# Kernel tuning notes

Hardware: AMD Instinct MI355X
Metric: run time of the kernel (lower is better)

## Reference

```python
import jax, jax.numpy as jnp
import numpy as np

B, L, D, H, FF, NS = 4, 1024, 1024, 16, 4096, 64
HD = D // H
EPS = 1e-5


def layer_norm(x, g, b):
    mu = jnp.mean(x, axis=-1, keepdims=True)
    var = jnp.mean(jnp.square(x - mu), axis=-1, keepdims=True)
    return (x - mu) * jax.lax.rsqrt(var + EPS) * g + b


def mha(xq, xkv, wqkv, bqkv, wo, bo, bias=None):
    # torch nn.MultiheadAttention with packed in_proj: rows [0:D]=Q, [D:2D]=K, [2D:3D]=V
    Bq, Lq, Dm = xq.shape
    q = (xq @ wqkv[:Dm].T + bqkv[:Dm]).reshape(Bq, Lq, H, HD).transpose(0, 2, 1, 3)
    k = (xkv @ wqkv[Dm:2 * Dm].T + bqkv[Dm:2 * Dm]).reshape(Bq, -1, H, HD).transpose(0, 2, 1, 3)
    v = (xkv @ wqkv[2 * Dm:].T + bqkv[2 * Dm:]).reshape(Bq, -1, H, HD).transpose(0, 2, 1, 3)
    scores = jnp.einsum('bhqd,bhkd->bhqk', q, k) / np.sqrt(HD).astype(np.float32)
    if bias is not None:
        scores = scores + bias.reshape(Bq, H, Lq, -1)
    attn = jax.nn.softmax(scores, axis=-1)
    out = jnp.einsum('bhqk,bhkd->bhqd', attn, v).transpose(0, 2, 1, 3).reshape(Bq, Lq, Dm)
    return out @ wo.T + bo


def setup_inputs() -> dict:
    key = jax.random.key(0)
    ks = jax.random.split(key, 16)
    w = lambda k, shape: jax.random.normal(k, shape, jnp.float32) * 0.02
    return {
        'x': jax.random.normal(ks[0], (B, L, D), jnp.float32),
        'alibi_bias': jax.random.normal(ks[1], (B * H, L, L), jnp.float32) * 0.1,
        'species_emb': jax.random.normal(ks[2], (B, NS, D), jnp.float32),
        'norm1_g': jnp.ones(D), 'norm1_b': jnp.zeros(D),
        'sa_wqkv': w(ks[3], (3 * D, D)), 'sa_bqkv': jnp.zeros(3 * D),
        'sa_wo': w(ks[4], (D, D)), 'sa_bo': jnp.zeros(D),
        'ca_nq_g': jnp.ones(D), 'ca_nq_b': jnp.zeros(D),
        'ca_nkv_g': jnp.ones(D), 'ca_nkv_b': jnp.zeros(D),
        'ca_wqkv': w(ks[5], (3 * D, D)), 'ca_bqkv': jnp.zeros(3 * D),
        'ca_wo': w(ks[6], (D, D)), 'ca_bo': jnp.zeros(D),
        'gate_param': jnp.float32(0.1),
        'ffn_g': jnp.ones(D), 'ffn_b': jnp.zeros(D),
        'ffn_w1': w(ks[7], (2 * FF, D)), 'ffn_b1': jnp.zeros(2 * FF),
        'ffn_w2': w(ks[8], (D, FF)), 'ffn_b2': jnp.zeros(D),
    }


def reference(x, alibi_bias, species_emb,
              norm1_g, norm1_b, sa_wqkv, sa_bqkv, sa_wo, sa_bo,
              ca_nq_g, ca_nq_b, ca_nkv_g, ca_nkv_b, ca_wqkv, ca_bqkv, ca_wo, ca_bo,
              gate_param, ffn_g, ffn_b, ffn_w1, ffn_b1, ffn_w2, ffn_b2):
    # 1) pre-norm self-attention with ALiBi additive bias
    h = layer_norm(x, norm1_g, norm1_b)
    h = mha(h, h, sa_wqkv, sa_bqkv, sa_wo, sa_bo, bias=alibi_bias)
    x = x + h  # dropout is identity in eval mode
    # 2) gated cross-attention with species embeddings
    q = layer_norm(x, ca_nq_g, ca_nq_b)
    kv = layer_norm(species_emb, ca_nkv_g, ca_nkv_b)
    cross = mha(q, kv, ca_wqkv, ca_bqkv, ca_wo, ca_bo)
    x = x + jax.nn.sigmoid(gate_param) * cross
    # 3) GEGLU feed-forward
    f = layer_norm(x, ffn_g, ffn_b) @ ffn_w1.T + ffn_b1
    val, gate = f[..., :FF], f[..., FF:]
    f = (val * jax.nn.gelu(gate, approximate=False)) @ ffn_w2.T + ffn_b2
    return x + f
```

## Files before the change

kernel.cpp:

```cpp
#include <hip/hip_runtime.h>
#include <hip/hip_bf16.h>
#include <cstdint>

#define DEVI __device__ __forceinline__

typedef __attribute__((ext_vector_type(8))) short  short8;
typedef __attribute__((ext_vector_type(8))) __bf16 bf16x8;
typedef __attribute__((ext_vector_type(4))) float  f32x4;

DEVI float bf2f(short s) {
    unsigned u = ((unsigned)(unsigned short)s) << 16;
    return __builtin_bit_cast(float, u);
}
DEVI short f2bf(float f) {
    unsigned u = __builtin_bit_cast(unsigned, f);
    u = u + 0x7FFF + ((u >> 16) & 1);
    return (short)(u >> 16);
}

__global__ __launch_bounds__(256) void cvt_bf16(const float* src, short* dst, long n) {
    const long i = ((long)blockIdx.x * 256 + threadIdx.x) * 8;
    const float4 a = *(const float4*)&src[i];
    const float4 b = *(const float4*)&src[i + 4];
    short8 o;
    o[0] = f2bf(a.x); o[1] = f2bf(a.y); o[2] = f2bf(a.z); o[3] = f2bf(a.w);
    o[4] = f2bf(b.x); o[5] = f2bf(b.y); o[6] = f2bf(b.z); o[7] = f2bf(b.w);
    *(short8*)&dst[i] = o;
}

struct GArgs {
    const short* A; long lda, sAb, sAh;
    const short* B; long ldb, sBb, sBh;
    short* C;       long ldc, sCb, sCh;
    const float* bias;
    const float* addm; long ldad, sDb, sDh;
    float* resid;
    float* outf;
    const float* gate;
    const float* addf;
    float scale;
    int K, nh;
};

template<int BM, int BN, int EPI>
__global__ __launch_bounds__(256) void gemm_bt(GArgs a) {
    constexpr int WM = BM / 2, WN = BN / 2, MI = WM / 16, NI = WN / 16;
    __shared__ __align__(16) short As[BM * 32];
    __shared__ __align__(16) short Bs[BN * 32];
    const int tid = threadIdx.x;
    const int wave = tid >> 6, lane = tid & 63;
    const int wm = (wave >> 1) * WM, wn = (wave & 1) * WN;
    const int q = lane >> 4, r = lane & 15;
    const long bb = blockIdx.z / a.nh, hh = blockIdx.z % a.nh;
    const short* Ab = a.A + bb * a.sAb + hh * a.sAh + (long)blockIdx.y * BM * a.lda;
    const short* Bb = a.B + bb * a.sBb + hh * a.sBh + (long)blockIdx.x * BN * a.ldb;
    const int trow = tid >> 2;
    const int tcol = (tid & 3) * 8;
    f32x4 acc[MI][NI] = {};

    for (int k0 = 0; k0 < a.K; k0 += 32) {
        __syncthreads();
#pragma unroll
        for (int i = 0; i < BM / 64; i++) {
            const short* g = Ab + (long)(i * 64 + trow) * a.lda + k0 + tcol;
            __builtin_amdgcn_global_load_lds(
                (const __attribute__((address_space(1))) void*)g,
                (__attribute__((address_space(3))) void*)&As[(i * 64 + trow) * 32 + tcol],
                16, 0, 0);
        }
#pragma unroll
        for (int i = 0; i < BN / 64; i++) {
            const short* g = Bb + (long)(i * 64 + trow) * a.ldb + k0 + tcol;
            __builtin_amdgcn_global_load_lds(
                (const __attribute__((address_space(1))) void*)g,
                (__attribute__((address_space(3))) void*)&Bs[(i * 64 + trow) * 32 + tcol],
                16, 0, 0);
        }
        asm volatile("s_waitcnt vmcnt(0)" ::: "memory");
        __syncthreads();
        bf16x8 av[MI], bv[NI];
#pragma unroll
        for (int mi = 0; mi < MI; mi++)
            av[mi] = __builtin_bit_cast(bf16x8, *(const short8*)&As[(wm + mi * 16 + r) * 32 + q * 8]);
#pragma unroll
        for (int ni = 0; ni < NI; ni++)
            bv[ni] = __builtin_bit_cast(bf16x8, *(const short8*)&Bs[(wn + ni * 16 + r) * 32 + q * 8]);
#pragma unroll
        for (int mi = 0; mi < MI; mi++)
#pragma unroll
            for (int ni = 0; ni < NI; ni++)
                acc[mi][ni] = __builtin_amdgcn_mfma_f32_16x16x32_bf16(av[mi], bv[ni], acc[mi][ni], 0, 0, 0);
    }

    const long m0 = (long)blockIdx.y * BM + wm;
    const long n0 = (long)blockIdx.x * BN + wn;
    float gs = a.scale;
    if (EPI == 2 && a.gate) gs *= 1.f / (1.f + __expf(-(*a.gate)));
#pragma unroll
    for (int mi = 0; mi < MI; mi++)
#pragma unroll
        for (int ni = 0; ni < NI; ni++)
#pragma unroll
            for (int j = 0; j < 4; j++) {
                const long m = m0 + mi * 16 + q * 4 + j;
                const long n = n0 + ni * 16 + r;
                float v = acc[mi][ni][j];
                if constexpr (EPI == 0) {
                    if (a.bias) v += a.bias[n];
                    a.C[bb * a.sCb + hh * a.sCh + m * a.ldc + n] = f2bf(v);
                } else if constexpr (EPI == 1) {
                    v *= a.scale;
                    if (a.addm) v += a.addm[bb * a.sDb + hh * a.sDh + m * a.ldad + n];
                    a.C[bb * a.sCb + hh * a.sCh + m * a.ldc + n] = f2bf(v);
                } else if constexpr (EPI == 2) {
                    if (a.bias) v += a.bias[n];
                    const long idx = m * a.ldc + n;
                    const float base = a.addf ? a.addf[idx] : a.resid[idx];
                    a.resid[idx] = base + gs * v;
                } else {
                    if (a.bias) v += a.bias[n];
                    a.outf[m * a.ldc + n] = a.resid[m * a.ldc + n] + v;
                }
            }
}

__global__ __launch_bounds__(256) void flash_sa(const short* qkv, const short* vt,
                                                const float* alibi, short* Obuf) {
    __shared__ __align__(16) short Qs[64 * 64], Ks[64 * 64], Vs[64 * 64], Ps[64 * 64];
    const int tid = threadIdx.x;
    const int wave = tid >> 6, lane = tid & 63, q = lane >> 4, r = lane & 15;
    const int qt = blockIdx.x, bh = blockIdx.y, b = bh >> 4, h = bh & 15;
    const long qrow0 = (long)b * 1024 + qt * 64;
    const int rw = tid >> 3, sp = tid & 7;

#pragma unroll
    for (int i = 0; i < 2; i++) {
        const int row = i * 32 + rw;
        const int c8 = (sp ^ (row & 7)) * 8;
        const short* g = qkv + (qrow0 + row) * 3072 + h * 64 + c8;
        __builtin_amdgcn_global_load_lds(
            (const __attribute__((address_space(1))) void*)g,
            (__attribute__((address_space(3))) void*)&Qs[row * 64 + sp * 8], 16, 0, 0);
    }

    f32x4 o[4] = {};
    float m_run[4], l_run[4];
#pragma unroll
    for (int j = 0; j < 4; j++) { m_run[j] = -1e30f; l_run[j] = 0.f; }

    for (int kt = 0; kt < 16; kt++) {
        __syncthreads();
#pragma unroll
        for (int i = 0; i < 2; i++) {
            const int row = i * 32 + rw;
            const int c8 = (sp ^ (row & 7)) * 8;
            const short* gk = qkv + ((long)b * 1024 + kt * 64 + row) * 3072 + 1024 + h * 64 + c8;
            __builtin_amdgcn_global_load_lds(
                (const __attribute__((address_space(1))) void*)gk,
                (__attribute__((address_space(3))) void*)&Ks[row * 64 + sp * 8], 16, 0, 0);
            const short* gv = vt + ((long)bh * 64 + row) * 1024 + kt * 64 + c8;
            __builtin_amdgcn_global_load_lds(
                (const __attribute__((address_space(1))) void*)gv,
                (__attribute__((address_space(3))) void*)&Vs[row * 64 + sp * 8], 16, 0, 0);
        }
        float al[4][4];
        const float* ab = alibi + (long)bh * 1048576 + (long)(qt * 64 + wave * 16) * 1024 + kt * 64;
#pragma unroll
        for (int ni = 0; ni < 4; ni++)
#pragma unroll
            for (int j = 0; j < 4; j++)
                al[ni][j] = ab[(q * 4 + j) * 1024 + ni * 16 + r];
        asm volatile("s_waitcnt vmcnt(0)" ::: "memory");
        __syncthreads();

        f32x4 sacc[4] = {};
        const int arow = wave * 16 + r;
#pragma unroll
        for (int kk = 0; kk < 2; kk++) {
            const bf16x8 av = __builtin_bit_cast(bf16x8,
                *(const short8*)&Qs[arow * 64 + (((kk * 4 + q) ^ (arow & 7)) * 8)]);
#pragma unroll
            for (int ni = 0; ni < 4; ni++) {
                const int brow = ni * 16 + r;
                const bf16x8 bv = __builtin_bit_cast(bf16x8,
                    *(const short8*)&Ks[brow * 64 + (((kk * 4 + q) ^ (brow & 7)) * 8)]);
                sacc[ni] = __builtin_amdgcn_mfma_f32_16x16x32_bf16(av, bv, sacc[ni], 0, 0, 0);
            }
        }
        float s[4][4];
#pragma unroll
        for (int ni = 0; ni < 4; ni++)
#pragma unroll
            for (int j = 0; j < 4; j++)
                s[ni][j] = sacc[ni][j] * 0.125f + al[ni][j];

        float p[4][4];
#pragma unroll
        for (int j = 0; j < 4; j++) {
            float mx = fmaxf(fmaxf(s[0][j], s[1][j]), fmaxf(s[2][j], s[3][j]));
#pragma unroll
            for (int off = 8; off; off >>= 1) mx = fmaxf(mx, __shfl_xor(mx, off));
            const float newm = fmaxf(m_run[j], mx);
            const float sc = __expf(m_run[j] - newm);
            m_run[j] = newm;
            float rs = 0.f;
#pragma unroll
            for (int ni = 0; ni < 4; ni++) { p[ni][j] = __expf(s[ni][j] - newm); rs += p[ni][j]; }
#pragma unroll
            for (int off = 8; off; off >>= 1) rs += __shfl_xor(rs, off);
            l_run[j] = l_run[j] * sc + rs;
#pragma unroll
            for (int nd = 0; nd < 4; nd++) o[nd][j] *= sc;
        }

#pragma unroll
        for (int ni = 0; ni < 4; ni++)
#pragma unroll
            for (int j = 0; j < 4; j++) {
                const int row = wave * 16 + q * 4 + j;
                const int col = ni * 16 + r;
                const int scol = (((col >> 3) ^ (row & 7)) << 3) | (col & 7);
                Ps[row * 64 + scol] = f2bf(p[ni][j]);
            }
        asm volatile("s_waitcnt lgkmcnt(0)" ::: "memory");

        const int prow = wave * 16 + r;
#pragma unroll
        for (int kk = 0; kk < 2; kk++) {
            const bf16x8 pa = __builtin_bit_cast(bf16x8,
                *(const short8*)&Ps[prow * 64 + (((kk * 4 + q) ^ (prow & 7)) * 8)]);
#pragma unroll
            for (int nd = 0; nd < 4; nd++) {
                const int vrow = nd * 16 + r;
                const bf16x8 vv = __builtin_bit_cast(bf16x8,
                    *(const short8*)&Vs[vrow * 64 + (((kk * 4 + q) ^ (vrow & 7)) * 8)]);
                o[nd] = __builtin_amdgcn_mfma_f32_16x16x32_bf16(pa, vv, o[nd], 0, 0, 0);
            }
        }
    }

#pragma unroll
    for (int nd = 0; nd < 4; nd++)
#pragma unroll
        for (int j = 0; j < 4; j++) {
            const long m = qrow0 + wave * 16 + q * 4 + j;
            Obuf[m * 1024 + h * 64 + nd * 16 + r] = f2bf(o[nd][j] / l_run[j]);
        }
}

__global__ __launch_bounds__(256) void ln_rows(const float* X, const float* gw,
                                               const float* bw, short* Y) {
    const long row = blockIdx.x;
    const float* x = X + row * 1024;
    const int t = threadIdx.x;
    float v[4], s1 = 0.f, s2 = 0.f;
#pragma unroll
    for (int i = 0; i < 4; i++) {
        v[i] = x[t + i * 256];
        s1 += v[i]; s2 += v[i] * v[i];
    }
#pragma unroll
    for (int o = 32; o; o >>= 1) { s1 += __shfl_xor(s1, o); s2 += __shfl_xor(s2, o); }
    __shared__ float sm[8];
    if ((t & 63) == 0) { sm[t >> 6] = s1; sm[4 + (t >> 6)] = s2; }
    __syncthreads();
    s1 = sm[0] + sm[1] + sm[2] + sm[3];
    s2 = sm[4] + sm[5] + sm[6] + sm[7];
    const float mu = s1 * (1.f / 1024.f);
    const float var = s2 * (1.f / 1024.f) - mu * mu;
    const float rr = rsqrtf(var + 1e-5f);
#pragma unroll
    for (int i = 0; i < 4; i++) {
        const int c = t + i * 256;
        Y[row * 1024 + c] = f2bf((v[i] - mu) * rr * gw[c] + bw[c]);
    }
}

__global__ __launch_bounds__(256) void softmax1024(short* S) {
    const long row = blockIdx.x;
    short* p = S + row * 1024;
    const int t = threadIdx.x;
    float v[4];
#pragma unroll
    for (int i = 0; i < 4; i++) v[i] = bf2f(p[t + i * 256]);
    float m = fmaxf(fmaxf(v[0], v[1]), fmaxf(v[2], v[3]));
#pragma unroll
    for (int o = 32; o; o >>= 1) m = fmaxf(m, __shfl_xor(m, o));
    __shared__ float sm[4];
    if ((t & 63) == 0) sm[t >> 6] = m;
    __syncthreads();
    m = fmaxf(fmaxf(sm[0], sm[1]), fmaxf(sm[2], sm[3]));
    float e[4], s = 0.f;
#pragma unroll
    for (int i = 0; i < 4; i++) { e[i] = __expf(v[i] - m); s += e[i]; }
#pragma unroll
    for (int o = 32; o; o >>= 1) s += __shfl_xor(s, o);
    __syncthreads();
    if ((t & 63) == 0) sm[t >> 6] = s;
    __syncthreads();
    s = sm[0] + sm[1] + sm[2] + sm[3];
    const float inv = 1.f / s;
#pragma unroll
    for (int i = 0; i < 4; i++) p[t + i * 256] = f2bf(e[i] * inv);
}

__global__ __launch_bounds__(256) void softmax64(short* S) {
    const long row = (long)blockIdx.x * 4 + (threadIdx.x >> 6);
    const int lane = threadIdx.x & 63;
    short* p = S + row * 64;
    float v = bf2f(p[lane]);
    float m = v;
#pragma unroll
    for (int o = 32; o; o >>= 1) m = fmaxf(m, __shfl_xor(m, o));
    float e = __expf(v - m), s = e;
#pragma unroll
    for (int o = 32; o; o >>= 1) s += __shfl_xor(s, o);
    p[lane] = f2bf(e / s);
}

__global__ __launch_bounds__(256) void transpose_v_sa(const short* qkv, short* vt) {
    __shared__ short tbuf[64][68];
    const int j0 = blockIdx.x * 64, h = blockIdx.y, b = blockIdx.z;
    const int tid = threadIdx.x;
#pragma unroll
    for (int i = 0; i < 16; i++) {
        const int idx = i * 256 + tid, jj = idx >> 6, hd = idx & 63;
        tbuf[jj][hd] = qkv[(long)(b * 1024 + j0 + jj) * 3072 + 2048 + h * 64 + hd];
    }
    __syncthreads();
    const long bh = b * 16 + h;
#pragma unroll
    for (int i = 0; i < 16; i++) {
        const int idx = i * 256 + tid, hd = idx >> 6, jj = idx & 63;
        vt[(bh * 64 + hd) * 1024 + j0 + jj] = tbuf[jj][hd];
    }
}

__global__ __launch_bounds__(256) void transpose_v_ca(const short* kv2, short* vt2) {
    __shared__ short tbuf[64][68];
    const int bh = blockIdx.x, b = bh >> 4, h = bh & 15;
    const int tid = threadIdx.x;
#pragma unroll
    for (int i = 0; i < 16; i++) {
        const int idx = i * 256 + tid, jj = idx >> 6, hd = idx & 63;
        tbuf[jj][hd] = kv2[(long)(b * 64 + jj) * 2048 + 1024 + h * 64 + hd];
    }
    __syncthreads();
#pragma unroll
    for (int i = 0; i < 16; i++) {
        const int idx = i * 256 + tid, hd = idx >> 6, jj = idx & 63;
        vt2[((long)bh * 64 + hd) * 64 + jj] = tbuf[jj][hd];
    }
}

__global__ __launch_bounds__(256) void geglu_inplace(short* f1) {
    const long i = (long)blockIdx.x * 256 + threadIdx.x;
    const long m = i >> 9, j8 = (i & 511) * 8;
    const short8 av = *(const short8*)&f1[m * 8192 + j8];
    const short8 gv = *(const short8*)&f1[m * 8192 + 4096 + j8];
    short8 o;
#pragma unroll
    for (int jj = 0; jj < 8; jj++) {
        const float xv = bf2f(av[jj]), gg = bf2f(gv[jj]);
        const float ge = 0.5f * gg * (1.f + erff(gg * 0.7071067811865476f));
        o[jj] = f2bf(xv * ge);
    }
    *(short8*)&f1[m * 8192 + j8] = o;
}

extern "C" void kernel_launch(void* const* d_in, const int* in_sizes, int n_in,
                              void* d_out, int out_size, void* d_ws, size_t ws_size,
                              hipStream_t stream) {
    const float* x        = (const float*)d_in[0];
    const float* alibi    = (const float*)d_in[1];
    const float* species  = (const float*)d_in[2];
    const float* n1g      = (const float*)d_in[3];
    const float* n1b      = (const float*)d_in[4];
    const float* sa_wqkv  = (const float*)d_in[5];
    const float* sa_bqkv  = (const float*)d_in[6];
    const float* sa_wo    = (const float*)d_in[7];
    const float* sa_bo    = (const float*)d_in[8];
    const float* ca_nq_g  = (const float*)d_in[9];
    const float* ca_nq_b  = (const float*)d_in[10];
    const float* ca_nkv_g = (const float*)d_in[11];
    const float* ca_nkv_b = (const float*)d_in[12];
    const float* ca_wqkv  = (const float*)d_in[13];
    const float* ca_bqkv  = (const float*)d_in[14];
    const float* ca_wo    = (const float*)d_in[15];
    const float* ca_bo    = (const float*)d_in[16];
    const float* gate     = (const float*)d_in[17];
    const float* ffn_g    = (const float*)d_in[18];
    const float* ffn_b    = (const float*)d_in[19];
    const float* ffn_w1   = (const float*)d_in[20];
    const float* ffn_b1   = (const float*)d_in[21];
    const float* ffn_w2   = (const float*)d_in[22];
    const float* ffn_b2   = (const float*)d_in[23];
    float* out = (float*)d_out;

    const dim3 blk(256);
    char* ws = (char*)d_ws;

    if (ws_size >= (304ull << 20)) {
        float* resid  = (float*)(ws);
        short* lnbuf  = (short*)(ws + (16l << 20));
        short* Obuf   = (short*)(ws + (24l << 20));
        short* vt     = (short*)(ws + (32l << 20));
        short* qkv    = (short*)(ws + (40l << 20));
        short* w_saq  = (short*)(ws + (64l << 20));
        short* w_sawo = (short*)(ws + (70l << 20));
        short* w_caq  = (short*)(ws + (72l << 20));
        short* w_cawo = (short*)(ws + (78l << 20));
        short* w_f1   = (short*)(ws + (80l << 20));
        short* w_f2   = (short*)(ws + (96l << 20));
        short* kv2    = (short*)(ws + (104l << 20));
        short* Sbuf   = (short*)(ws + (112l << 20));
        short* f1     = (short*)(ws + (240l << 20));

        cvt_bf16<<<1536, blk, 0, stream>>>(sa_wqkv, w_saq, 3145728);
        cvt_bf16<<<512,  blk, 0, stream>>>(sa_wo,   w_sawo, 1048576);
        cvt_bf16<<<1536, blk, 0, stream>>>(ca_wqkv, w_caq, 3145728);
        cvt_bf16<<<512,  blk, 0, stream>>>(ca_wo,   w_cawo, 1048576);
        cvt_bf16<<<4096, blk, 0, stream>>>(ffn_w1,  w_f1, 8388608);
        cvt_bf16<<<2048, blk, 0, stream>>>(ffn_w2,  w_f2, 4194304);

        ln_rows<<<4096, blk, 0, stream>>>(x, n1g, n1b, lnbuf);

        {
            GArgs a{}; a.A = lnbuf; a.lda = 1024; a.B = w_saq; a.ldb = 1024;
            a.C = qkv; a.ldc = 3072; a.bias = sa_bqkv; a.K = 1024; a.nh = 1; a.scale = 1.f;
            gemm_bt<128, 128, 0><<<dim3(24, 32, 1), blk, 0, stream>>>(a);
        }
        transpose_v_sa<<<dim3(16, 16, 4), blk, 0, stream>>>(qkv, vt);

        flash_sa<<<dim3(16, 64), blk, 0, stream>>>(qkv, vt, alibi, Obuf);

        {
            GArgs a{}; a.A = Obuf; a.lda = 1024; a.B = w_sawo; a.ldb = 1024;
            a.ldc = 1024; a.bias = sa_bo; a.resid = resid; a.addf = x;
            a.scale = 1.f; a.K = 1024; a.nh = 1;
            gemm_bt<128, 64, 2><<<dim3(16, 32, 1), blk, 0, stream>>>(a);
        }

        ln_rows<<<4096, blk, 0, stream>>>(resid, ca_nq_g, ca_nq_b, lnbuf);
        {
            GArgs a{}; a.A = lnbuf; a.lda = 1024; a.B = w_caq; a.ldb = 1024;
            a.C = qkv; a.ldc = 1024; a.bias = ca_bqkv; a.K = 1024; a.nh = 1; a.scale = 1.f;
            gemm_bt<128, 64, 0><<<dim3(16, 32, 1), blk, 0, stream>>>(a);
        }
        ln_rows<<<256, blk, 0, stream>>>(species, ca_nkv_g, ca_nkv_b, lnbuf);
        {
            GArgs a{}; a.A = lnbuf; a.lda = 1024; a.B = w_caq + 1024 * 1024; a.ldb = 1024;
            a.C = kv2; a.ldc = 2048; a.bias = ca_bqkv + 1024; a.K = 1024; a.nh = 1; a.scale = 1.f;
            gemm_bt<128, 128, 0><<<dim3(16, 2, 1), blk, 0, stream>>>(a);
        }
        transpose_v_ca<<<64, blk, 0, stream>>>(kv2, vt);
        {
            GArgs a{}; a.A = qkv; a.lda = 1024; a.sAb = 1048576; a.sAh = 64;
            a.B = kv2; a.ldb = 2048; a.sBb = 131072; a.sBh = 64;
            a.C = Sbuf; a.ldc = 64; a.sCb = 1048576; a.sCh = 65536;
            a.scale = 0.125f; a.K = 64; a.nh = 16;
            gemm_bt<64, 64, 1><<<dim3(1, 16, 64), blk, 0, stream>>>(a);
        }
        softmax64<<<16384, blk, 0, stream>>>(Sbuf);
        {
            GArgs a{}; a.A = Sbuf; a.lda = 64; a.sAb = 1048576; a.sAh = 65536;
            a.B = vt; a.ldb = 64; a.sBb = 65536; a.sBh = 4096;
            a.C = Obuf; a.ldc = 1024; a.sCb = 1048576; a.sCh = 64;
            a.K = 64; a.nh = 16; a.scale = 1.f;
            gemm_bt<64, 64, 0><<<dim3(1, 16, 64), blk, 0, stream>>>(a);
        }
        {
            GArgs a{}; a.A = Obuf; a.lda = 1024; a.B = w_cawo; a.ldb = 1024;
            a.ldc = 1024; a.bias = ca_bo; a.resid = resid; a.gate = gate;
            a.scale = 1.f; a.K = 1024; a.nh = 1;
            gemm_bt<128, 64, 2><<<dim3(16, 32, 1), blk, 0, stream>>>(a);
        }

        ln_rows<<<4096, blk, 0, stream>>>(resid, ffn_g, ffn_b, lnbuf);
        {
            GArgs a{}; a.A = lnbuf; a.lda = 1024; a.B = w_f1; a.ldb = 1024;
            a.C = f1; a.ldc = 8192; a.bias = ffn_b1; a.K = 1024; a.nh = 1; a.scale = 1.f;
            gemm_bt<128, 128, 0><<<dim3(64, 32, 1), blk, 0, stream>>>(a);
        }
        geglu_inplace<<<8192, blk, 0, stream>>>(f1);
        {
            GArgs a{}; a.A = f1; a.lda = 8192; a.B = w_f2; a.ldb = 4096;
            a.ldc = 1024; a.bias = ffn_b2; a.resid = resid; a.outf = out;
            a.scale = 1.f; a.K = 4096; a.nh = 1;
            gemm_bt<128, 64, 3><<<dim3(16, 32, 1), blk, 0, stream>>>(a);
        }
        return;
    }

    float* resid  = (float*)(ws);
    short* lnbuf  = (short*)(ws + (16l << 20));
    short* Obuf   = (short*)(ws + (24l << 20));
    short* vt     = (short*)(ws + (32l << 20));
    short* qkv    = (short*)(ws + (40l << 20));
    short* Sbuf   = (short*)(ws + (64l << 20));
    short* f1     = Sbuf;
    short* kv2    = qkv + 4194304;
    short* w_sawo = (short*)(ws + (80l << 20));
    short* w_caq  = (short*)(ws + (82l << 20));
    short* w_cawo = (short*)(ws + (88l << 20));
    short* w_saq  = (short*)(ws + (90l << 20));
    short* w_f1   = qkv;
    short* w_f2   = (short*)(ws + (56l << 20));

    cvt_bf16<<<1536, blk, 0, stream>>>(sa_wqkv, w_saq, 3145728);
    cvt_bf16<<<512,  blk, 0, stream>>>(sa_wo,   w_sawo, 1048576);
    cvt_bf16<<<1536, blk, 0, stream>>>(ca_wqkv, w_caq, 3145728);
    cvt_bf16<<<512,  blk, 0, stream>>>(ca_wo,   w_cawo, 1048576);

    hipMemcpyAsync(resid, x, (size_t)4194304 * 4, hipMemcpyDeviceToDevice, stream);
    ln_rows<<<4096, blk, 0, stream>>>(x, n1g, n1b, lnbuf);

    {
        GArgs a{}; a.A = lnbuf; a.lda = 1024; a.B = w_saq; a.ldb = 1024;
        a.C = qkv; a.ldc = 3072; a.bias = sa_bqkv; a.K = 1024; a.nh = 1; a.scale = 1.f;
        gemm_bt<128, 128, 0><<<dim3(24, 32, 1), blk, 0, stream>>>(a);
    }
    transpose_v_sa<<<dim3(16, 16, 4), blk, 0, stream>>>(qkv, vt);

    for (int c = 0; c < 8; c++) {
        const int b = c >> 1, hc = c & 1;
        const long boff = (long)b * 1024 * 3072;
        {
            GArgs a{}; a.A = qkv + boff + hc * 512; a.lda = 3072; a.sAh = 64;
            a.B = qkv + boff + 1024 + hc * 512; a.ldb = 3072; a.sBh = 64;
            a.C = Sbuf; a.ldc = 1024; a.sCh = 1048576;
            a.addm = alibi + ((long)(b * 16 + hc * 8)) * 1048576; a.ldad = 1024; a.sDh = 1048576;
            a.scale = 0.125f; a.K = 64; a.nh = 8;
            gemm_bt<128, 128, 1><<<dim3(8, 8, 8), blk, 0, stream>>>(a);
        }
        softmax1024<<<8192, blk, 0, stream>>>(Sbuf);
        {
            GArgs a{}; a.A = Sbuf; a.lda = 1024; a.sAh = 1048576;
            a.B = vt + (long)b * 1048576 + (long)hc * 8 * 65536; a.ldb = 1024; a.sBh = 65536;
            a.C = Obuf + (long)b * 1048576 + hc * 512; a.ldc = 1024; a.sCh = 64;
            a.K = 1024; a.nh = 8; a.scale = 1.f;
            gemm_bt<64, 64, 0><<<dim3(1, 16, 8), blk, 0, stream>>>(a);
        }
    }
    {
        GArgs a{}; a.A = Obuf; a.lda = 1024; a.B = w_sawo; a.ldb = 1024;
        a.ldc = 1024; a.bias = sa_bo; a.resid = resid; a.scale = 1.f; a.K = 1024; a.nh = 1;
        gemm_bt<128, 128, 2><<<dim3(8, 32, 1), blk, 0, stream>>>(a);
    }

    ln_rows<<<4096, blk, 0, stream>>>(resid, ca_nq_g, ca_nq_b, lnbuf);
    {
        GArgs a{}; a.A = lnbuf; a.lda = 1024; a.B = w_caq; a.ldb = 1024;
        a.C = qkv; a.ldc = 1024; a.bias = ca_bqkv; a.K = 1024; a.nh = 1; a.scale = 1.f;
        gemm_bt<128, 128, 0><<<dim3(8, 32, 1), blk, 0, stream>>>(a);
    }
    ln_rows<<<256, blk, 0, stream>>>(species, ca_nkv_g, ca_nkv_b, lnbuf);
    {
        GArgs a{}; a.A = lnbuf; a.lda = 1024; a.B = w_caq + 1024 * 1024; a.ldb = 1024;
        a.C = kv2; a.ldc = 2048; a.bias = ca_bqkv + 1024; a.K = 1024; a.nh = 1; a.scale = 1.f;
        gemm_bt<128, 128, 0><<<dim3(16, 2, 1), blk, 0, stream>>>(a);
    }
    transpose_v_ca<<<64, blk, 0, stream>>>(kv2, vt);
    {
        GArgs a{}; a.A = qkv; a.lda = 1024; a.sAb = 1048576; a.sAh = 64;
        a.B = kv2; a.ldb = 2048; a.sBb = 131072; a.sBh = 64;
        a.C = Sbuf; a.ldc = 64; a.sCb = 1048576; a.sCh = 65536;
        a.scale = 0.125f; a.K = 64; a.nh = 16;
        gemm_bt<64, 64, 1><<<dim3(1, 16, 64), blk, 0, stream>>>(a);
    }
    cvt_bf16<<<4096, blk, 0, stream>>>(ffn_w1, w_f1, 8388608);
    cvt_bf16<<<2048, blk, 0, stream>>>(ffn_w2, w_f2, 4194304);

    softmax64<<<16384, blk, 0, stream>>>(Sbuf);
    {
        GArgs a{}; a.A = Sbuf; a.lda = 64; a.sAb = 1048576; a.sAh = 65536;
        a.B = vt; a.ldb = 64; a.sBb = 65536; a.sBh = 4096;
        a.C = Obuf; a.ldc = 1024; a.sCb = 1048576; a.sCh = 64;
        a.K = 64; a.nh = 16; a.scale = 1.f;
        gemm_bt<64, 64, 0><<<dim3(1, 16, 64), blk, 0, stream>>>(a);
    }
    {
        GArgs a{}; a.A = Obuf; a.lda = 1024; a.B = w_cawo; a.ldb = 1024;
        a.ldc = 1024; a.bias = ca_bo; a.resid = resid; a.gate = gate;
        a.scale = 1.f; a.K = 1024; a.nh = 1;
        gemm_bt<128, 128, 2><<<dim3(8, 32, 1), blk, 0, stream>>>(a);
    }

    ln_rows<<<4096, blk, 0, stream>>>(resid, ffn_g, ffn_b, lnbuf);
    for (int rc = 0; rc < 2; rc++) {
        const long ro = (long)rc * 2048;
        {
            GArgs a{}; a.A = lnbuf + ro * 1024; a.lda = 1024; a.B = w_f1; a.ldb = 1024;
            a.C = f1; a.ldc = 8192; a.bias = ffn_b1; a.K = 1024; a.nh = 1; a.scale = 1.f;
            gemm_bt<128, 128, 0><<<dim3(64, 16, 1), blk, 0, stream>>>(a);
        }
        geglu_inplace<<<4096, blk, 0, stream>>>(f1);
        {
            GArgs a{}; a.A = f1; a.lda = 8192; a.B = w_f2; a.ldb = 4096;
            a.ldc = 1024; a.bias = ffn_b2; a.resid = resid + ro * 1024; a.outf = out + ro * 1024;
            a.scale = 1.f; a.K = 4096; a.nh = 1;
            gemm_bt<128, 128, 3><<<dim3(8, 16, 1), blk, 0, stream>>>(a);
        }
    }
}
```

Baseline: 980.7 us.

## Fuse GEGLU into FFN1 GEMM, fuse cross-attention, remap block order

FFN1 now runs in a dedicated GEMM that computes the value and gate tiles together and applies the exact-erf GELU product in the epilogue. This removes the 8192-wide f1 intermediate and the separate geglu pass. The three-kernel cross-attention path (score GEMM, softmax, PV GEMM) becomes a single flash_ca kernel, since there are only 64 keys, so the score matrix never reaches global memory. Block indices in the GEMMs and flash_sa are also remapped with an XCD-style permutation to improve L2 locality. The cost is more accumulator registers in the fused GEMM, which may lower occupancy.

```diff
diff --git a/kernel.cpp b/kernel.cpp
--- a/kernel.cpp
+++ b/kernel.cpp
@@ -51,9 +51,13 @@
     const int wave = tid >> 6, lane = tid & 63;
     const int wm = (wave >> 1) * WM, wn = (wave & 1) * WN;
     const int q = lane >> 4, r = lane & 15;
+    const int gx = gridDim.x, gy = gridDim.y;
+    int flat = (int)(blockIdx.y * gx + blockIdx.x);
+    { const int cp = (gx * gy) >> 3; flat = (flat & 7) * cp + (flat >> 3); }
+    const int bx = flat % gx, by = flat / gx;
     const long bb = blockIdx.z / a.nh, hh = blockIdx.z % a.nh;
-    const short* Ab = a.A + bb * a.sAb + hh * a.sAh + (long)blockIdx.y * BM * a.lda;
-    const short* Bb = a.B + bb * a.sBb + hh * a.sBh + (long)blockIdx.x * BN * a.ldb;
+    const short* Ab = a.A + bb * a.sAb + hh * a.sAh + (long)by * BM * a.lda;
+    const short* Bb = a.B + bb * a.sBb + hh * a.sBh + (long)bx * BN * a.ldb;
     const int trow = tid >> 2;
     const int tcol = (tid & 3) * 8;
     f32x4 acc[MI][NI] = {};
@@ -92,8 +96,8 @@
                 acc[mi][ni] = __builtin_amdgcn_mfma_f32_16x16x32_bf16(av[mi], bv[ni], acc[mi][ni], 0, 0, 0);
     }
 
-    const long m0 = (long)blockIdx.y * BM + wm;
-    const long n0 = (long)blockIdx.x * BN + wn;
+    const long m0 = (long)by * BM + wm;
+    const long n0 = (long)bx * BN + wn;
     float gs = a.scale;
     if (EPI == 2 && a.gate) gs *= 1.f / (1.f + __expf(-(*a.gate)));
 #pragma unroll
@@ -124,12 +128,97 @@
             }
 }
 
+struct GGArgs {
+    const short* A; long lda;
+    const short* Bv; const short* Bg; long ldb;
+    short* C; long ldc;
+    const float* b1;
+    int K;
+};
+__global__ __launch_bounds__(256) void gemm_geglu(GGArgs a) {
+    constexpr int BM = 128, BN = 64, WM = 64, WN = 32, MI = 4, NI = 2;
+    __shared__ __align__(16) short As[BM * 32];
+    __shared__ __align__(16) short Bs[BN * 32];
+    __shared__ __align__(16) short Gs[BN * 32];
+    const int tid = threadIdx.x;
+    const int wave = tid >> 6, lane = tid & 63;
+    const int wm = (wave >> 1) * WM, wn = (wave & 1) * WN;
+    const int q = lane >> 4, r = lane & 15;
+    const int gx = gridDim.x, gy = gridDim.y;
+    int flat = (int)(blockIdx.y * gx + blockIdx.x);
+    { const int cp = (gx * gy) >> 3; flat = (flat & 7) * cp + (flat >> 3); }
+    const int bx = flat % gx, by = flat / gx;
+    const short* Ab = a.A + (long)by * BM * a.lda;
+    const short* Bb = a.Bv + (long)bx * BN * a.ldb;
+    const short* Gb = a.Bg + (long)bx * BN * a.ldb;
+    const int trow = tid >> 2, tcol = (tid & 3) * 8;
+    f32x4 accv[MI][NI] = {}, accg[MI][NI] = {};
+
+    for (int k0 = 0; k0 < a.K; k0 += 32) {
+        __syncthreads();
+#pragma unroll
+        for (int i = 0; i < 2; i++) {
+            const short* g = Ab + (long)(i * 64 + trow) * a.lda + k0 + tcol;
+            __builtin_amdgcn_global_load_lds(
+                (const __attribute__((address_space(1))) void*)g,
+                (__attribute__((address_space(3))) void*)&As[(i * 64 + trow) * 32 + tcol],
+                16, 0, 0);
+        }
+        {
+            const short* g = Bb + (long)trow * a.ldb + k0 + tcol;
+            __builtin_amdgcn_global_load_lds(
+                (const __attribute__((address_space(1))) void*)g,
+                (__attribute__((address_space(3))) void*)&Bs[trow * 32 + tcol], 16, 0, 0);
+            const short* g2 = Gb + (long)trow * a.ldb + k0 + tcol;
+            __builtin_amdgcn_global_load_lds(
+                (const __attribute__((address_space(1))) void*)g2,
+                (__attribute__((address_space(3))) void*)&Gs[trow * 32 + tcol], 16, 0, 0);
+        }
+        asm volatile("s_waitcnt vmcnt(0)" ::: "memory");
+        __syncthreads();
+        bf16x8 av[MI], bv[NI], gv[NI];
+#pragma unroll
+        for (int mi = 0; mi < MI; mi++)
+            av[mi] = __builtin_bit_cast(bf16x8, *(const short8*)&As[(wm + mi * 16 + r) * 32 + q * 8]);
+#pragma unroll
+        for (int ni = 0; ni < NI; ni++) {
+            bv[ni] = __builtin_bit_cast(bf16x8, *(const short8*)&Bs[(wn + ni * 16 + r) * 32 + q * 8]);
+            gv[ni] = __builtin_bit_cast(bf16x8, *(const short8*)&Gs[(wn + ni * 16 + r) * 32 + q * 8]);
+        }
+#pragma unroll
+        for (int mi = 0; mi < MI; mi++)
+#pragma unroll
+            for (int ni = 0; ni < NI; ni++) {
+                accv[mi][ni] = __builtin_amdgcn_mfma_f32_16x16x32_bf16(av[mi], bv[ni], accv[mi][ni], 0, 0, 0);
+                accg[mi][ni] = __builtin_amdgcn_mfma_f32_16x16x32_bf16(av[mi], gv[ni], accg[mi][ni], 0, 0, 0);
+            }
+    }
+
+    const long m0 = (long)by * BM + wm;
+    const long n0 = (long)bx * BN + wn;
+#pragma unroll
+    for (int mi = 0; mi < MI; mi++)
+#pragma unroll
+        for (int ni = 0; ni < NI; ni++)
+#pragma unroll
+            for (int j = 0; j < 4; j++) {
+                const long m = m0 + mi * 16 + q * 4 + j;
+                const long n = n0 + ni * 16 + r;
+                const float v = accv[mi][ni][j] + a.b1[n];
+                const float g = accg[mi][ni][j] + a.b1[4096 + n];
+                const float ge = 0.5f * g * (1.f + erff(g * 0.7071067811865476f));
+                a.C[m * a.ldc + n] = f2bf(v * ge);
+            }
+}
+
 __global__ __launch_bounds__(256) void flash_sa(const short* qkv, const short* vt,
                                                 const float* alibi, short* Obuf) {
     __shared__ __align__(16) short Qs[64 * 64], Ks[64 * 64], Vs[64 * 64], Ps[64 * 64];
     const int tid = threadIdx.x;
     const int wave = tid >> 6, lane = tid & 63, q = lane >> 4, r = lane & 15;
-    const int qt = blockIdx.x, bh = blockIdx.y, b = bh >> 4, h = bh & 15;
+    int flat = (int)(blockIdx.y * 16 + blockIdx.x);
+    flat = (flat & 7) * 128 + (flat >> 3);
+    const int qt = flat & 15, bh = flat >> 4, b = bh >> 4, h = bh & 15;
     const long qrow0 = (long)b * 1024 + qt * 64;
     const int rw = tid >> 3, sp = tid & 7;
 
@@ -245,6 +334,100 @@
         for (int j = 0; j < 4; j++) {
             const long m = qrow0 + wave * 16 + q * 4 + j;
             Obuf[m * 1024 + h * 64 + nd * 16 + r] = f2bf(o[nd][j] / l_run[j]);
+        }
+}
+
+__global__ __launch_bounds__(256) void flash_ca(const short* q2, const short* kv2,
+                                                const short* vt, short* Obuf) {
+    __shared__ __align__(16) short Qs[64 * 64], Ks[64 * 64], Vs[64 * 64], Ps[64 * 64];
+    const int tid = threadIdx.x;
+    const int wave = tid >> 6, lane = tid & 63, q = lane >> 4, r = lane & 15;
+    int flat = (int)(blockIdx.y * 16 + blockIdx.x);
+    flat = (flat & 7) * 128 + (flat >> 3);
+    const int qt = flat & 15, bh = flat >> 4, b = bh >> 4, h = bh & 15;
+    const long qrow0 = (long)b * 1024 + qt * 64;
+    const int rw = tid >> 3, sp = tid & 7;
+
+#pragma unroll
+    for (int i = 0; i < 2; i++) {
+        const int row = i * 32 + rw;
+        const int c8 = (sp ^ (row & 7)) * 8;
+        const short* gq = q2 + (qrow0 + row) * 1024 + h * 64 + c8;
+        __builtin_amdgcn_global_load_lds(
+            (const __attribute__((address_space(1))) void*)gq,
+            (__attribute__((address_space(3))) void*)&Qs[row * 64 + sp * 8], 16, 0, 0);
+        const short* gk = kv2 + ((long)b * 64 + row) * 2048 + h * 64 + c8;
+        __builtin_amdgcn_global_load_lds(
+            (const __attribute__((address_space(1))) void*)gk,
+            (__attribute__((address_space(3))) void*)&Ks[row * 64 + sp * 8], 16, 0, 0);
+        const short* gv = vt + ((long)bh * 64 + row) * 64 + c8;
+        __builtin_amdgcn_global_load_lds(
+            (const __attribute__((address_space(1))) void*)gv,
+            (__attribute__((address_space(3))) void*)&Vs[row * 64 + sp * 8], 16, 0, 0);
+    }
+    asm volatile("s_waitcnt vmcnt(0)" ::: "memory");
+    __syncthreads();
+
+    f32x4 sacc[4] = {};
+    const int arow = wave * 16 + r;
+#pragma unroll
+    for (int kk = 0; kk < 2; kk++) {
+        const bf16x8 av = __builtin_bit_cast(bf16x8,
+            *(const short8*)&Qs[arow * 64 + (((kk * 4 + q) ^ (arow & 7)) * 8)]);
+#pragma unroll
+        for (int ni = 0; ni < 4; ni++) {
+            const int brow = ni * 16 + r;
+            const bf16x8 bv = __builtin_bit_cast(bf16x8,
+                *(const short8*)&Ks[brow * 64 + (((kk * 4 + q) ^ (brow & 7)) * 8)]);
+            sacc[ni] = __builtin_amdgcn_mfma_f32_16x16x32_bf16(av, bv, sacc[ni], 0, 0, 0);
+        }
+    }
+    float p[4][4], linv[4];
+#pragma unroll
+    for (int j = 0; j < 4; j++) {
+        float s0 = sacc[0][j] * 0.125f, s1 = sacc[1][j] * 0.125f;
+        float s2 = sacc[2][j] * 0.125f, s3 = sacc[3][j] * 0.125f;
+        float mx = fmaxf(fmaxf(s0, s1), fmaxf(s2, s3));
+#pragma unroll
+        for (int off = 8; off; off >>= 1) mx = fmaxf(mx, __shfl_xor(mx, off));
+        p[0][j] = __expf(s0 - mx); p[1][j] = __expf(s1 - mx);
+        p[2][j] = __expf(s2 - mx); p[3][j] = __expf(s3 - mx);
+        float rs = p[0][j] + p[1][j] + p[2][j] + p[3][j];
+#pragma unroll
+        for (int off = 8; off; off >>= 1) rs += __shfl_xor(rs, off);
+        linv[j] = 1.f / rs;
+    }
+#pragma unroll
+    for (int ni = 0; ni < 4; ni++)
+#pragma unroll
+        for (int j = 0; j < 4; j++) {
+            const int row = wave * 16 + q * 4 + j;
+            const int col = ni * 16 + r;
+            const int scol = (((col >> 3) ^ (row & 7)) << 3) | (col & 7);
+            Ps[row * 64 + scol] = f2bf(p[ni][j]);
+        }
+    asm volatile("s_waitcnt lgkmcnt(0)" ::: "memory");
+
+    f32x4 o[4] = {};
+    const int prow = wave * 16 + r;
+#pragma unroll
+    for (int kk = 0; kk < 2; kk++) {
+        const bf16x8 pa = __builtin_bit_cast(bf16x8,
+            *(const short8*)&Ps[prow * 64 + (((kk * 4 + q) ^ (prow & 7)) * 8)]);
+#pragma unroll
+        for (int nd = 0; nd < 4; nd++) {
+            const int vrow = nd * 16 + r;
+            const bf16x8 vv = __builtin_bit_cast(bf16x8,
+                *(const short8*)&Vs[vrow * 64 + (((kk * 4 + q) ^ (vrow & 7)) * 8)]);
+            o[nd] = __builtin_amdgcn_mfma_f32_16x16x32_bf16(pa, vv, o[nd], 0, 0, 0);
+        }
+    }
+#pragma unroll
+    for (int nd = 0; nd < 4; nd++)
+#pragma unroll
+        for (int j = 0; j < 4; j++) {
+            const long m = qrow0 + wave * 16 + q * 4 + j;
+            Obuf[m * 1024 + h * 64 + nd * 16 + r] = f2bf(o[nd][j] * linv[j]);
         }
 }
 
@@ -413,8 +596,7 @@
         short* w_f1   = (short*)(ws + (80l << 20));
         short* w_f2   = (short*)(ws + (96l << 20));
         short* kv2    = (short*)(ws + (104l << 20));
-        short* Sbuf   = (short*)(ws + (112l << 20));
-        short* f1     = (short*)(ws + (240l << 20));
+        short* g1     = (short*)(ws + (240l << 20));
 
         cvt_bf16<<<1536, blk, 0, stream>>>(sa_wqkv, w_saq, 3145728);
         cvt_bf16<<<512,  blk, 0, stream>>>(sa_wo,   w_sawo, 1048576);
@@ -454,21 +636,9 @@
             gemm_bt<128, 128, 0><<<dim3(16, 2, 1), blk, 0, stream>>>(a);
         }
         transpose_v_ca<<<64, blk, 0, stream>>>(kv2, vt);
-        {
-            GArgs a{}; a.A = qkv; a.lda = 1024; a.sAb = 1048576; a.sAh = 64;
-            a.B = kv2; a.ldb = 2048; a.sBb = 131072; a.sBh = 64;
-            a.C = Sbuf; a.ldc = 64; a.sCb = 1048576; a.sCh = 65536;
-            a.scale = 0.125f; a.K = 64; a.nh = 16;
-            gemm_bt<64, 64, 1><<<dim3(1, 16, 64), blk, 0, stream>>>(a);
-        }
-        softmax64<<<16384, blk, 0, stream>>>(Sbuf);
-        {
-            GArgs a{}; a.A = Sbuf; a.lda = 64; a.sAb = 1048576; a.sAh = 65536;
-            a.B = vt; a.ldb = 64; a.sBb = 65536; a.sBh = 4096;
-            a.C = Obuf; a.ldc = 1024; a.sCb = 1048576; a.sCh = 64;
-            a.K = 64; a.nh = 16; a.scale = 1.f;
-            gemm_bt<64, 64, 0><<<dim3(1, 16, 64), blk, 0, stream>>>(a);
-        }
+
+        flash_ca<<<dim3(16, 64), blk, 0, stream>>>(qkv, kv2, vt, Obuf);
+
         {
             GArgs a{}; a.A = Obuf; a.lda = 1024; a.B = w_cawo; a.ldb = 1024;
             a.ldc = 1024; a.bias = ca_bo; a.resid = resid; a.gate = gate;
@@ -478,13 +648,13 @@
 
         ln_rows<<<4096, blk, 0, stream>>>(resid, ffn_g, ffn_b, lnbuf);
         {
-            GArgs a{}; a.A = lnbuf; a.lda = 1024; a.B = w_f1; a.ldb = 1024;
-            a.C = f1; a.ldc = 8192; a.bias = ffn_b1; a.K = 1024; a.nh = 1; a.scale = 1.f;
-            gemm_bt<128, 128, 0><<<dim3(64, 32, 1), blk, 0, stream>>>(a);
-        }
-        geglu_inplace<<<8192, blk, 0, stream>>>(f1);
-        {
-            GArgs a{}; a.A = f1; a.lda = 8192; a.B = w_f2; a.ldb = 4096;
+            GGArgs a{}; a.A = lnbuf; a.lda = 1024;
+            a.Bv = w_f1; a.Bg = w_f1 + (long)4096 * 1024; a.ldb = 1024;
+            a.C = g1; a.ldc = 4096; a.b1 = ffn_b1; a.K = 1024;
+            gemm_geglu<<<dim3(64, 32, 1), blk, 0, stream>>>(a);
+        }
+        {
+            GArgs a{}; a.A = g1; a.lda = 4096; a.B = w_f2; a.ldb = 4096;
             a.ldc = 1024; a.bias = ffn_b2; a.resid = resid; a.outf = out;
             a.scale = 1.f; a.K = 4096; a.nh = 1;
             gemm_bt<128, 64, 3><<<dim3(16, 32, 1), blk, 0, stream>>>(a);
```

Measured after the change: 928.9 us. 5.3% less time.
